# Kernel tuning notes

Measured on AMD Instinct MI355X. Metric: run time of the kernel, lower is better.

The kernel has to match this reference:

```python
import jax, jax.numpy as jnp
import numpy as np

S = 64        # num_states
ODIM = 8      # padded neighbor-feature width
H = 256       # HIDDEN_DIM
A = 16        # num_actions
B = 16384     # batch (dtpt)
IDIM = S + ODIM
NEG_SLOPE = 0.01  # nn.LeakyReLU default
EPS = 1e-5        # nn.LayerNorm default


def setup_inputs() -> dict:
    key = jax.random.key(0)
    ks = jax.random.split(key, 8)
    x = jax.random.normal(ks[0], (B, S), jnp.float32)
    # per-state neighbor indices into x's feature dim, padded to ODIM with a mask
    o_idx = jax.random.randint(ks[1], (S, ODIM), 0, S)
    o_len = jax.random.randint(ks[2], (S,), 1, ODIM + 1)
    o_mask = jnp.arange(ODIM)[None, :] < o_len[:, None]  # [S, ODIM] bool

    def lin(k, fin, fout):
        bound = 1.0 / np.sqrt(fin)
        kw, kb = jax.random.split(k)
        W = jax.random.uniform(kw, (S, fin, fout), jnp.float32, -bound, bound)
        b = jax.random.uniform(kb, (S, fout), jnp.float32, -bound, bound)
        return W, b

    W1, b1 = lin(ks[3], IDIM, H)
    W2, b2 = lin(ks[4], H, H)
    Wp, bp = lin(ks[5], H, A)
    g1 = jnp.ones((S, H), jnp.float32); be1 = jnp.zeros((S, H), jnp.float32)
    g2 = jnp.ones((S, H), jnp.float32); be2 = jnp.zeros((S, H), jnp.float32)
    return dict(x=x, o_idx=o_idx, o_mask=o_mask, W1=W1, b1=b1, g1=g1, be1=be1,
                W2=W2, b2=b2, g2=g2, be2=be2, Wp=Wp, bp=bp)


def _layer_norm(h, g, b):
    # h: [B, S, H], per-state affine params g,b: [S, H]
    mu = jnp.mean(h, axis=-1, keepdims=True)
    var = jnp.mean((h - mu) ** 2, axis=-1, keepdims=True)
    return (h - mu) * jax.lax.rsqrt(var + EPS) * g[None] + b[None]


def reference(x, o_idx, o_mask, W1, b1, g1, be1, W2, b2, g2, be2, Wp, bp):
    # irregular gather: for each state s take x[:, o_nbr_index[s]], zero-pad to ODIM
    o = jnp.where(o_mask[None, :, :], x[:, o_idx], jnp.float32(0))  # [B, S, ODIM]
    one_hot = jnp.broadcast_to(jnp.eye(S, dtype=x.dtype)[None], (x.shape[0], S, S))
    inp = jnp.concatenate([one_hot, o], axis=-1)  # [B, S, IDIM]

    h = jnp.einsum('bsi,sih->bsh', inp, W1) + b1[None]
    h = _layer_norm(jax.nn.leaky_relu(h, NEG_SLOPE), g1, be1)
    h = jnp.einsum('bsh,shk->bsk', h, W2) + b2[None]
    h = _layer_norm(jax.nn.leaky_relu(h, NEG_SLOPE), g2, be2)
    pi_logit = jnp.einsum('bsh,sha->bsa', h, Wp) + bp[None]  # [B, S, A]
    lg_sm = jax.nn.log_softmax(pi_logit, axis=-1)
    return pi_logit, lg_sm
```

## Files before the change

### kernel.cpp

```cpp
#include <hip/hip_runtime.h>

#define LNEPS 1e-5f

typedef __attribute__((ext_vector_type(8)))  short          bf16x8;
typedef __attribute__((ext_vector_type(8)))  unsigned short u16x8;
typedef __attribute__((ext_vector_type(4)))  float          f32x4;
typedef __attribute__((ext_vector_type(16))) float          f32x16;
typedef __attribute__((ext_vector_type(4)))  unsigned int   u32x4;

#define MFMA32(a, b, c) __builtin_amdgcn_mfma_f32_32x32x16_bf16((a), (b), (c), 0, 0, 0)

#define WS_W2G  0
#define WS_A1   8388608
#define WS_WPG  8912896
#define WS_UC2  10027008
#define WS_MIDX 10092544

union U8 { bf16x8 v; unsigned u[4]; };

__device__ __forceinline__ unsigned short f2bf(float v) {
  union { float f; unsigned u; } a; a.f = v;
  unsigned r = a.u + 0x7fffu + ((a.u >> 16) & 1u);
  return (unsigned short)(r >> 16);
}
__device__ __forceinline__ unsigned cvtpk(float lo, float hi) {
  unsigned r;
  asm("v_cvt_pk_bf16_f32 %0, %1, %2" : "=v"(r) : "v"(lo), "v"(hi));
  return r;
}
__device__ __forceinline__ void swap2(unsigned& a, unsigned& b) {
  asm volatile("v_permlane32_swap_b32 %0, %1" : "+v"(a), "+v"(b));
}
__device__ __forceinline__ void plswap(unsigned w, unsigned& lo, unsigned& hi) {
  unsigned a = w, b = w;
  asm volatile("v_permlane32_swap_b32 %0, %1" : "+v"(a), "+v"(b));
  lo = a; hi = b;
}

__global__ void prep_midx_k(const int* __restrict__ oidx,
                            const unsigned* __restrict__ mask32,
                            int* __restrict__ midx) {
  __shared__ int fgt1, ffl;
  const int t = threadIdx.x;
  if (t == 0) { fgt1 = 0; ffl = 0; }
  __syncthreads();
  if (t < 128) {
    unsigned wv = mask32[t];
    if (wv == 0x3f800000u) atomicOr(&ffl, 1);
    else if (wv > 1u)      atomicOr(&fgt1, 1);
  }
  __syncthreads();
  const int mode = ffl ? 2 : (fgt1 ? 1 : 0);
  int mv;
  if (mode == 2)      mv = (((const float*)mask32)[t] != 0.0f) ? 1 : 0;
  else if (mode == 1) mv = (int)((const unsigned char*)mask32)[t];
  else                mv = ((const int*)mask32)[t];
  midx[t] = (mv != 0) ? oidx[t] : -1;
}

__global__ __launch_bounds__(256) void prep_w2g_k(
    const float* __restrict__ W2, const float* __restrict__ g1,
    unsigned short* __restrict__ w2g) {
  const int tid = blockIdx.x * 256 + threadIdx.x;
  const int l = tid & 63;
  const int t = (tid >> 6) & 15;
  const int i = (tid >> 10) & 7;
  const int s = tid >> 13;
  const int n = i * 32 + (l & 31);
  const int h = l >> 5;
  const float* w = W2 + (size_t)s * 65536;
  const float* g = g1 + s * 256;
  u16x8 v;
#pragma unroll
  for (int j = 0; j < 8; ++j) {
    const int k = t * 16 + h * 8 + j;
    v[j] = f2bf(w[k * 256 + n] * g[k]);
  }
  ((u16x8*)w2g)[tid] = v;
}

__global__ __launch_bounds__(256) void prep_uc2_k(
    const float* __restrict__ W2, const float* __restrict__ g1,
    const float* __restrict__ be1, const float* __restrict__ b2,
    unsigned* __restrict__ uc2) {
  const int tid = blockIdx.x * 256 + threadIdx.x;
  const int s = tid >> 8, n = tid & 255;
  const float* w = W2 + (size_t)s * 65536 + n;
  const float* g = g1 + s * 256;
  const float* be = be1 + s * 256;
  float u = 0.f, c = 0.f;
#pragma unroll 8
  for (int k = 0; k < 256; ++k) {
    const float wk = w[k * 256];
    u = fmaf(wk, g[k], u);
    c = fmaf(wk, be[k], c);
  }
  c += b2[tid];
  uc2[tid] = (unsigned)f2bf(u) | ((unsigned)f2bf(c) << 16);
}

__global__ __launch_bounds__(256) void prep_a1_k(
    const float* __restrict__ W1, const float* __restrict__ b1,
    unsigned short* __restrict__ a1b) {
  const int tid = blockIdx.x * 256 + threadIdx.x;
  const int l = tid & 63;
  const int i = (tid >> 6) & 7;
  const int s = tid >> 9;
  const int n = i * 32 + (l & 31);
  const float* w = W1 + (size_t)s * 72 * 256;
  u16x8 v;
#pragma unroll
  for (int j = 0; j < 8; ++j) v[j] = 0;
  if (l < 32) {
#pragma unroll
    for (int j = 0; j < 8; ++j) v[j] = f2bf(w[(64 + j) * 256 + n]);
  } else {
    v[0] = f2bf(w[s * 256 + n] + b1[s * 256 + n]);
  }
  ((u16x8*)a1b)[tid] = v;
}

__global__ __launch_bounds__(256) void prep_wpg_k(
    const float* __restrict__ Wp, const float* __restrict__ g2,
    const float* __restrict__ be2, const float* __restrict__ bp,
    unsigned short* __restrict__ wpg) {
  const int tid = blockIdx.x * 256 + threadIdx.x;
  const int l = tid & 63;
  const int r = tid >> 6;
  const int t = r % 17;
  const int s = r / 17;
  const int a = l & 31;
  const int h = l >> 5;
  u16x8 v;
#pragma unroll
  for (int j = 0; j < 8; ++j) v[j] = 0;
  if (t < 16) {
    if (a < 16) {
      const float* w = Wp + (size_t)s * 4096;
      const float* g = g2 + s * 256;
#pragma unroll
      for (int j = 0; j < 8; ++j) {
        const int k = t * 16 + h * 8 + j;
        v[j] = f2bf(w[k * 16 + a] * g[k]);
      }
    }
  } else if (h == 0 && a < 16) {
    const float* w = Wp + (size_t)s * 4096;
    float up = 0.f, cp = 0.f;
#pragma unroll 8
    for (int k = 0; k < 256; ++k) {
      const float wk = w[k * 16 + a];
      up = fmaf(wk, g2[s * 256 + k], up);
      cp = fmaf(wk, be2[s * 256 + k], cp);
    }
    cp += bp[s * 16 + a];
    v[0] = f2bf(up); v[1] = f2bf(cp);
  }
  ((u16x8*)wpg)[tid] = v;
}

__device__ __forceinline__ void pack_tile(const f32x16& a,
                                          unsigned* f0, unsigned* f1) {
  unsigned w0 = cvtpk(a[0], a[1]),   w1 = cvtpk(a[2], a[3]);
  unsigned w2 = cvtpk(a[4], a[5]),   w3 = cvtpk(a[6], a[7]);
  unsigned w4 = cvtpk(a[8], a[9]),   w5 = cvtpk(a[10], a[11]);
  unsigned w6 = cvtpk(a[12], a[13]), w7 = cvtpk(a[14], a[15]);
  swap2(w0, w2); swap2(w1, w3); swap2(w4, w6); swap2(w5, w7);
  f0[0] = w0; f0[1] = w1; f0[2] = w2; f0[3] = w3;
  f1[0] = w4; f1[1] = w5; f1[2] = w6; f1[3] = w7;
}

__global__ __launch_bounds__(512, 2) void actor_main(
    const float* __restrict__ x, const int* __restrict__ midx,
    const unsigned short* __restrict__ w2g, const unsigned* __restrict__ uc2,
    const unsigned short* __restrict__ a1b, const unsigned short* __restrict__ wpg,
    float* __restrict__ out) {
  extern __shared__ char lds[];
  const int tid = threadIdx.x;
  const int wv = tid >> 6;
  const int l = tid & 63;
  const int bl = l & 31;
  const int h = l >> 5;
  const int s = blockIdx.x >> 2;
  const int rowstart = (blockIdx.x & 3) << 12;

  {
    const u32x4* src = (const u32x4*)(w2g + (size_t)s * 65536);
    u32x4* dst = (u32x4*)lds;
#pragma unroll
    for (int i = 0; i < 16; ++i) dst[i * 512 + tid] = src[i * 512 + tid];
  }

  unsigned aext[8];
#pragma unroll
  for (int i = 0; i < 8; ++i) {
    const unsigned t = uc2[(s * 8 + i) * 32 + bl];
    aext[i] = h ? 0u : t;
  }
  const int4 mi4 = ((const int4*)(midx + s * 8))[h];
  const bf16x8* A1 = ((const bf16x8*)a1b) + (size_t)(s * 8) * 64 + l;
  const bf16x8* A3 = ((const bf16x8*)wpg) + (size_t)(s * 17) * 64 + l;

  const float* xbase = x + (size_t)(rowstart + wv * 32 + bl) * 64;

  float ga = mi4.x < 0 ? 0.f : xbase[mi4.x];
  float gb = mi4.y < 0 ? 0.f : xbase[mi4.y];
  float gc = mi4.z < 0 ? 0.f : xbase[mi4.z];
  float gd = mi4.w < 0 ? 0.f : xbase[mi4.w];

  __syncthreads();

  for (int it = 0; it < 16; ++it) {
    const int row = rowstart + it * 256 + wv * 32 + bl;

    unsigned oa0, ob0, oa1, ob1;
    plswap(cvtpk(ga, gb), oa0, ob0);
    plswap(cvtpk(gc, gd), oa1, ob1);
    U8 B1;
    B1.u[0] = h ? 0x00003F80u : oa0;
    B1.u[1] = h ? 0u : oa1;
    B1.u[2] = h ? 0u : ob0;
    B1.u[3] = h ? 0u : ob1;

    {
      const float* xn = xbase + (size_t)(((it + 1) & 15) * 256) * 64;
      ga = mi4.x < 0 ? 0.f : xn[mi4.x];
      gb = mi4.y < 0 ? 0.f : xn[mi4.y];
      gc = mi4.z < 0 ? 0.f : xn[mi4.z];
      gd = mi4.w < 0 ? 0.f : xn[mi4.w];
    }

    f32x16 acc1[8];
#pragma unroll
    for (int i = 0; i < 8; ++i) {
      f32x16 z = {};
      acc1[i] = MFMA32(A1[i * 64], B1.v, z);
    }

    float s0 = 0.f, s1 = 0.f, q0 = 0.f, q1 = 0.f;
    unsigned yf[16][4];
#pragma unroll
    for (int i = 0; i < 8; ++i) {
#pragma unroll
      for (int r = 0; r < 16; ++r) {
        float v = acc1[i][r];
        v = fmaxf(v, 0.01f * v);
        acc1[i][r] = v;
        if (r & 1) { s1 += v; q1 = fmaf(v, v, q1); }
        else       { s0 += v; q0 = fmaf(v, v, q0); }
      }
      pack_tile(acc1[i], yf[2 * i], yf[2 * i + 1]);
    }
    float sum = s0 + s1, ssq = q0 + q1;
    sum += __shfl_xor(sum, 32, 64);
    ssq += __shfl_xor(ssq, 32, 64);
    const float m1 = sum * 0.00390625f;
    const float var1 = fmaf(ssq, 0.00390625f, -m1 * m1) + LNEPS;
    const float rho1 = rsqrtf(var1);
    const float std1 = var1 * rho1;
    const unsigned be2w = cvtpk(-m1, std1);

    f32x16 acc2[8];
#pragma unroll
    for (int i = 0; i < 8; ++i) { f32x16 z = {}; acc2[i] = z; }
#pragma unroll
    for (int t = 0; t < 16; ++t) {
      U8 Bf;
      Bf.u[0] = yf[t][0]; Bf.u[1] = yf[t][1]; Bf.u[2] = yf[t][2]; Bf.u[3] = yf[t][3];
      bf16x8 Af[8];
#pragma unroll
      for (int i = 0; i < 8; ++i)
        Af[i] = *(const bf16x8*)(lds + (((i << 4) + t) << 10) + (l << 4));
      __builtin_amdgcn_s_setprio(1);
#pragma unroll
      for (int i = 0; i < 8; ++i) acc2[i] = MFMA32(Af[i], Bf.v, acc2[i]);
      __builtin_amdgcn_s_setprio(0);
    }
    {
      U8 Bx; Bx.u[0] = h ? 0u : be2w; Bx.u[1] = 0; Bx.u[2] = 0; Bx.u[3] = 0;
#pragma unroll
      for (int i = 0; i < 8; ++i) {
        U8 Ax; Ax.u[0] = aext[i]; Ax.u[1] = 0; Ax.u[2] = 0; Ax.u[3] = 0;
        acc2[i] = MFMA32(Ax.v, Bx.v, acc2[i]);
      }
    }

    f32x16 a3a = {}, a3b = {};
    s0 = s1 = q0 = q1 = 0.f;
#pragma unroll
    for (int i = 0; i < 8; ++i) {
#pragma unroll
      for (int r = 0; r < 16; ++r) {
        float v = acc2[i][r];
        v = fmaxf(v, 0.01f * v);
        acc2[i][r] = v;
        if (r & 1) { s1 += v; q1 = fmaf(v, v, q1); }
        else       { s0 += v; q0 = fmaf(v, v, q0); }
      }
      U8 Bf0, Bf1;
      pack_tile(acc2[i], Bf0.u, Bf1.u);
      a3a = MFMA32(A3[(2 * i) * 64], Bf0.v, a3a);
      a3b = MFMA32(A3[(2 * i + 1) * 64], Bf1.v, a3b);
    }
    float sum2 = s0 + s1, ssq2 = q0 + q1;
    sum2 += __shfl_xor(sum2, 32, 64);
    ssq2 += __shfl_xor(ssq2, 32, 64);
    const float mp = sum2 * 0.00390625f;
    const float qp = ssq2 * 0.00390625f;
    const float var2 = rho1 * rho1 * fmaf(-mp, mp, qp) + LNEPS;
    const float rho2 = rsqrtf(var2);
    const float sigma = rho1 * rho2;
    const float inv = var2 * rho2 * std1;
    const unsigned be3w = cvtpk(-mp, inv);
    {
      U8 Bx; Bx.u[0] = h ? 0u : be3w; Bx.u[1] = 0; Bx.u[2] = 0; Bx.u[3] = 0;
      a3a = MFMA32(A3[16 * 64], Bx.v, a3a);
    }

    float lg[8];
#pragma unroll
    for (int r = 0; r < 8; ++r) lg[r] = sigma * (a3a[r] + a3b[r]);
    float mx = fmaxf(fmaxf(fmaxf(lg[0], lg[1]), fmaxf(lg[2], lg[3])),
                     fmaxf(fmaxf(lg[4], lg[5]), fmaxf(lg[6], lg[7])));
    mx = fmaxf(mx, __shfl_xor(mx, 32, 64));
    float es = 0.f;
#pragma unroll
    for (int r = 0; r < 8; ++r) es += __expf(lg[r] - mx);
    es += __shfl_xor(es, 32, 64);
    const float lse = mx + __logf(es);

    const size_t ob = (((size_t)row << 6) + s) * 16 + (h << 2);
    f32x4 v0 = {lg[0], lg[1], lg[2], lg[3]};
    f32x4 v1 = {lg[4], lg[5], lg[6], lg[7]};
    *(f32x4*)(out + ob) = v0;
    *(f32x4*)(out + ob + 8) = v1;
    f32x4 w0 = {lg[0] - lse, lg[1] - lse, lg[2] - lse, lg[3] - lse};
    f32x4 w1 = {lg[4] - lse, lg[5] - lse, lg[6] - lse, lg[7] - lse};
    *(f32x4*)(out + 16777216 + ob) = w0;
    *(f32x4*)(out + 16777216 + ob + 8) = w1;
  }
}

extern "C" void kernel_launch(void* const* d_in, const int* in_sizes, int n_in,
                              void* d_out, int out_size, void* d_ws, size_t ws_size,
                              hipStream_t stream) {
  const float* x    = (const float*)d_in[0];
  const int*   oidx = (const int*)d_in[1];
  const unsigned* omask = (const unsigned*)d_in[2];
  const float* W1 = (const float*)d_in[3];
  const float* b1 = (const float*)d_in[4];
  const float* g1 = (const float*)d_in[5];
  const float* be1 = (const float*)d_in[6];
  const float* W2 = (const float*)d_in[7];
  const float* b2 = (const float*)d_in[8];
  const float* g2 = (const float*)d_in[9];
  const float* be2 = (const float*)d_in[10];
  const float* Wp = (const float*)d_in[11];
  const float* bp = (const float*)d_in[12];
  float* out = (float*)d_out;

  char* ws = (char*)d_ws;
  unsigned short* wsW2G = (unsigned short*)(ws + WS_W2G);
  unsigned short* wsA1  = (unsigned short*)(ws + WS_A1);
  unsigned short* wsWPG = (unsigned short*)(ws + WS_WPG);
  unsigned*       wsUC2 = (unsigned*)(ws + WS_UC2);
  int*            wsMIDX = (int*)(ws + WS_MIDX);

  prep_midx_k<<<1, 512, 0, stream>>>(oidx, omask, wsMIDX);
  prep_w2g_k<<<2048, 256, 0, stream>>>(W2, g1, wsW2G);
  prep_uc2_k<<<64, 256, 0, stream>>>(W2, g1, be1, b2, wsUC2);
  prep_a1_k<<<128, 256, 0, stream>>>(W1, b1, wsA1);
  prep_wpg_k<<<272, 256, 0, stream>>>(Wp, g2, be2, bp, wsWPG);

  hipFuncSetAttribute((const void*)actor_main,
                      hipFuncAttributeMaxDynamicSharedMemorySize, 131072);
  actor_main<<<256, 512, 131072, stream>>>(
      x, wsMIDX, wsW2G, wsUC2, wsA1, wsWPG, out);
}
```

Baseline: 321.8 us.

## Interleave layer-1 epilogue with layer-2 MFMAs and software-pipeline weight loads

Layer 1's MFMA, LeakyReLU and statistics epilogue is now fused tile by tile with the layer-2 MFMA accumulation. Each packed 32-row tile feeds the layer-2 MFMAs immediately instead of first staging all 16 packed tiles in registers. LDS fragments for the next k-step and the global A1/A3 weight fragments are prefetched one step ahead, so load latency can overlap MFMA and VALU work. The aim is to cut register pressure from the yf staging array and raise overlap between the matrix and vector units. The setprio hints are dropped, and the double-buffered fragments add live registers.

```diff
diff --git a/kernel.cpp b/kernel.cpp
--- a/kernel.cpp
+++ b/kernel.cpp
@@ -200,6 +200,7 @@
   const int4 mi4 = ((const int4*)(midx + s * 8))[h];
   const bf16x8* A1 = ((const bf16x8*)a1b) + (size_t)(s * 8) * 64 + l;
   const bf16x8* A3 = ((const bf16x8*)wpg) + (size_t)(s * 17) * 64 + l;
+  const char* ldsl = lds + (l << 4);
 
   const float* xbase = x + (size_t)(rowstart + wv * 32 + bl) * 64;
 
@@ -230,27 +231,50 @@
       gd = mi4.w < 0 ? 0.f : xn[mi4.w];
     }
 
-    f32x16 acc1[8];
+    float s0 = 0.f, s1 = 0.f, q0 = 0.f, q1 = 0.f;
+    f32x16 acc2[8];
+    bf16x8 a1n = A1[0];
+    bf16x8 Afc[8];
+#pragma unroll
+    for (int j = 0; j < 8; ++j)
+      Afc[j] = *(const bf16x8*)(ldsl + ((j * 16 + 0) << 10));
+
 #pragma unroll
     for (int i = 0; i < 8; ++i) {
       f32x16 z = {};
-      acc1[i] = MFMA32(A1[i * 64], B1.v, z);
-    }
-
-    float s0 = 0.f, s1 = 0.f, q0 = 0.f, q1 = 0.f;
-    unsigned yf[16][4];
-#pragma unroll
-    for (int i = 0; i < 8; ++i) {
+      const f32x16 accP = MFMA32(a1n, B1.v, z);
+      if (i < 7) a1n = A1[(i + 1) * 64];
+
+      f32x16 yv;
 #pragma unroll
       for (int r = 0; r < 16; ++r) {
-        float v = acc1[i][r];
+        float v = accP[r];
         v = fmaxf(v, 0.01f * v);
-        acc1[i][r] = v;
+        yv[r] = v;
         if (r & 1) { s1 += v; q1 = fmaf(v, v, q1); }
         else       { s0 += v; q0 = fmaf(v, v, q0); }
       }
-      pack_tile(acc1[i], yf[2 * i], yf[2 * i + 1]);
-    }
+      U8 Bf0, Bf1;
+      pack_tile(yv, Bf0.u, Bf1.u);
+
+#pragma unroll
+      for (int j = 0; j < 8; ++j) {
+        if (i == 0) { f32x16 zz = {}; acc2[j] = MFMA32(Afc[j], Bf0.v, zz); }
+        else        { acc2[j] = MFMA32(Afc[j], Bf0.v, acc2[j]); }
+      }
+      bf16x8 Afn[8];
+#pragma unroll
+      for (int j = 0; j < 8; ++j)
+        Afn[j] = *(const bf16x8*)(ldsl + ((j * 16 + 2 * i + 1) << 10));
+#pragma unroll
+      for (int j = 0; j < 8; ++j) acc2[j] = MFMA32(Afn[j], Bf1.v, acc2[j]);
+      if (i < 7) {
+#pragma unroll
+        for (int j = 0; j < 8; ++j)
+          Afc[j] = *(const bf16x8*)(ldsl + ((j * 16 + 2 * i + 2) << 10));
+      }
+    }
+
     float sum = s0 + s1, ssq = q0 + q1;
     sum += __shfl_xor(sum, 32, 64);
     ssq += __shfl_xor(ssq, 32, 64);
@@ -259,23 +283,7 @@
     const float rho1 = rsqrtf(var1);
     const float std1 = var1 * rho1;
     const unsigned be2w = cvtpk(-m1, std1);
-
-    f32x16 acc2[8];
-#pragma unroll
-    for (int i = 0; i < 8; ++i) { f32x16 z = {}; acc2[i] = z; }
-#pragma unroll
-    for (int t = 0; t < 16; ++t) {
-      U8 Bf;
-      Bf.u[0] = yf[t][0]; Bf.u[1] = yf[t][1]; Bf.u[2] = yf[t][2]; Bf.u[3] = yf[t][3];
-      bf16x8 Af[8];
-#pragma unroll
-      for (int i = 0; i < 8; ++i)
-        Af[i] = *(const bf16x8*)(lds + (((i << 4) + t) << 10) + (l << 4));
-      __builtin_amdgcn_s_setprio(1);
-#pragma unroll
-      for (int i = 0; i < 8; ++i) acc2[i] = MFMA32(Af[i], Bf.v, acc2[i]);
-      __builtin_amdgcn_s_setprio(0);
-    }
+    bf16x8 p0 = A3[0], p1 = A3[64];
     {
       U8 Bx; Bx.u[0] = h ? 0u : be2w; Bx.u[1] = 0; Bx.u[2] = 0; Bx.u[3] = 0;
 #pragma unroll
@@ -289,18 +297,23 @@
     s0 = s1 = q0 = q1 = 0.f;
 #pragma unroll
     for (int i = 0; i < 8; ++i) {
+      bf16x8 n0, n1;
+      if (i < 7) { n0 = A3[(2 * i + 2) * 64]; n1 = A3[(2 * i + 3) * 64]; }
+      else       { n0 = A3[16 * 64]; n1 = p1; }
+      f32x16 yv;
 #pragma unroll
       for (int r = 0; r < 16; ++r) {
         float v = acc2[i][r];
         v = fmaxf(v, 0.01f * v);
-        acc2[i][r] = v;
+        yv[r] = v;
         if (r & 1) { s1 += v; q1 = fmaf(v, v, q1); }
         else       { s0 += v; q0 = fmaf(v, v, q0); }
       }
       U8 Bf0, Bf1;
-      pack_tile(acc2[i], Bf0.u, Bf1.u);
-      a3a = MFMA32(A3[(2 * i) * 64], Bf0.v, a3a);
-      a3b = MFMA32(A3[(2 * i + 1) * 64], Bf1.v, a3b);
+      pack_tile(yv, Bf0.u, Bf1.u);
+      a3a = MFMA32(p0, Bf0.v, a3a);
+      a3b = MFMA32(p1, Bf1.v, a3b);
+      p0 = n0; p1 = n1;
     }
     float sum2 = s0 + s1, ssq2 = q0 + q1;
     sum2 += __shfl_xor(sum2, 32, 64);
@@ -314,7 +327,7 @@
     const unsigned be3w = cvtpk(-mp, inv);
     {
       U8 Bx; Bx.u[0] = h ? 0u : be3w; Bx.u[1] = 0; Bx.u[2] = 0; Bx.u[3] = 0;
-      a3a = MFMA32(A3[16 * 64], Bx.v, a3a);
+      a3a = MFMA32(p0, Bx.v, a3a);
     }
 
     float lg[8];
```

Measured after the change: 272.3 us. -15.4%, faster.
